# Kernel optimization log

Measured on AMD Instinct MI355X. Metric: run time of the kernel, lower is better.

## Reference

```python
import jax, jax.numpy as jnp
import numpy as np

EPS = 1e-5
K = 3  # deformable conv kernel size


def _conv2d_same(x, w, b=None):
    # x (N,C,H,W), w (O,I,kh,kw), stride 1, SAME padding
    y = jax.lax.conv_general_dilated(
        x, w, window_strides=(1, 1), padding='SAME',
        dimension_numbers=('NCHW', 'OIHW', 'NCHW'))
    if b is not None:
        y = y + b[None, :, None, None]
    return y


def _bilinear_sample(x, ys, xs):
    # x (N,C,H,W); ys, xs (N,H,W) float sample coords -> (N,C,H,W), zero pad outside
    N, C, H, W = x.shape
    y0 = jnp.floor(ys)
    x0 = jnp.floor(xs)
    dy = ys - y0
    dx = xs - x0
    xf = x.reshape(N, C, H * W)

    def gather(yi, xi):
        valid = (yi >= 0) & (yi < H) & (xi >= 0) & (xi < W)
        yc = jnp.clip(yi, 0, H - 1).astype(jnp.int32)
        xc = jnp.clip(xi, 0, W - 1).astype(jnp.int32)
        idx = (yc * W + xc).reshape(N, 1, H * W)
        v = jnp.take_along_axis(xf, jnp.broadcast_to(idx, (N, C, H * W)), axis=2)
        return v.reshape(N, C, H, W) * valid[:, None].astype(x.dtype)

    v00 = gather(y0, x0)
    v01 = gather(y0, x0 + 1)
    v10 = gather(y0 + 1, x0)
    v11 = gather(y0 + 1, x0 + 1)
    dy = dy[:, None]
    dx = dx[:, None]
    return (v00 * (1 - dy) * (1 - dx) + v01 * (1 - dy) * dx
            + v10 * dy * (1 - dx) + v11 * dy * dx)


def _dcn_v2(x, w_off, b_off, w, b):
    # Modulated deformable conv (DCNv2), 3x3, stride 1, pad 1
    N, Cin, H, W = x.shape
    om = _conv2d_same(x, w_off, b_off)              # (N, 3*K*K, H, W)
    o1, o2, m = jnp.split(om, 3, axis=1)
    off = jnp.concatenate([o1, o2], axis=1)          # (N, 2*K*K, H, W)
    mask = jax.nn.sigmoid(m)                         # (N, K*K, H, W)
    base_y = jnp.arange(H, dtype=x.dtype)[None, :, None]  # (1,H,1)
    base_x = jnp.arange(W, dtype=x.dtype)[None, None, :]  # (1,1,W)
    out = jnp.broadcast_to(b[None, :, None, None], (N, w.shape[0], H, W)).astype(x.dtype)
    for k in range(K * K):  # fixed small loop over kernel taps
        ki, kj = k // K, k % K
        ys = base_y + (ki - 1) + off[:, 2 * k]
        xs = base_x + (kj - 1) + off[:, 2 * k + 1]
        v = _bilinear_sample(x, ys, xs) * mask[:, k][:, None]
        out = out + jnp.einsum('nchw,oc->nohw', v, w[:, :, ki, kj])
    return out


def _batchnorm(x, gamma, beta):
    # training-mode BN over (N,H,W)
    mu = x.mean(axis=(0, 2, 3), keepdims=True)
    var = x.var(axis=(0, 2, 3), keepdims=True)
    xhat = (x - mu) * jax.lax.rsqrt(var + EPS)
    return xhat * gamma[None, :, None, None] + beta[None, :, None, None]


def _conv_transpose2d(x, w):
    # torch ConvTranspose2d(k=4, s=2, p=1, bias=False); w (Cin, Cout, 4, 4)
    kernel = jnp.flip(w, (2, 3)).transpose(1, 0, 2, 3)  # (Cout, Cin, 4, 4)
    return jax.lax.conv_general_dilated(
        x, kernel, window_strides=(1, 1),
        padding=((2, 2), (2, 2)), lhs_dilation=(2, 2),
        dimension_numbers=('NCHW', 'OIHW', 'NCHW'))


def setup_inputs() -> dict:
    key = jax.random.key(0)
    ks = jax.random.split(key, 9)
    N, inC, outC, H, W = 8, 256, 256, 64, 64
    x = jax.random.normal(ks[0], (N, inC, H, W), dtype=jnp.float32)
    w_off = jax.random.normal(ks[1], (3 * K * K, inC, K, K), dtype=jnp.float32) * 0.01
    b_off = jnp.zeros((3 * K * K,), dtype=jnp.float32)
    w_dcn = jax.random.normal(ks[2], (outC, inC, K, K), dtype=jnp.float32) * (1.0 / np.sqrt(inC * K * K))
    b_dcn = jnp.zeros((outC,), dtype=jnp.float32)
    gamma1 = jnp.ones((outC,), dtype=jnp.float32)
    beta1 = jnp.zeros((outC,), dtype=jnp.float32)
    w_ct = jax.random.normal(ks[3], (outC, outC, 4, 4), dtype=jnp.float32) * (1.0 / np.sqrt(outC * 16))
    gamma2 = jnp.ones((outC,), dtype=jnp.float32)
    beta2 = jnp.zeros((outC,), dtype=jnp.float32)
    return {'x': x, 'w_off': w_off, 'b_off': b_off, 'w_dcn': w_dcn,
            'b_dcn': b_dcn, 'gamma1': gamma1, 'beta1': beta1,
            'w_ct': w_ct, 'gamma2': gamma2, 'beta2': beta2}


def reference(x, w_off, b_off, w_dcn, b_dcn, gamma1, beta1, w_ct, gamma2, beta2):
    out = _dcn_v2(x, w_off, b_off, w_dcn, b_dcn)
    out = jax.nn.relu(_batchnorm(out, gamma1, beta1))
    out = _conv_transpose2d(out, w_ct)
    out = jax.nn.relu(_batchnorm(out, gamma2, beta2))
    return out  # (N, outC, 2H, 2W)
```

## Files before the change

kernel.cpp:

```cpp
#include <hip/hip_runtime.h>


#define OFF_XT   0u
#define SZ_XT    (8u*64u*64u*256u)
#define OFF_Y1   (OFF_XT + SZ_XT)
#define SZ_Y1    SZ_XT
#define OFF_OM   (OFF_Y1 + SZ_Y1)
#define SZ_OM    (8u*27u*4096u)
#define OFF_WD   (OFF_OM + SZ_OM)
#define SZ_WD    (9u*256u*256u)
#define OFF_WC   (OFF_WD + SZ_WD)
#define SZ_WC    (16u*256u*256u)
#define OFF_WO   (OFF_WC + 524288u)
#define OFF_P1   (OFF_WC + 565248u)
#define OFF_ST   (OFF_WC + SZ_WC)

typedef __attribute__((ext_vector_type(8))) short bf16x8;
typedef __attribute__((ext_vector_type(4))) float f32x4;

__device__ __forceinline__ unsigned short f2bf(float f) {
  unsigned int u = __float_as_uint(f);
  u += 0x7fffu + ((u >> 16) & 1u);
  return (unsigned short)(u >> 16);
}

__device__ __forceinline__ unsigned int lerp_pair(unsigned int u00, unsigned int u01,
                                                  unsigned int u10, unsigned int u11,
                                                  float w0, float w1, float w2, float w3) {
  float lo = w0 * __uint_as_float(u00 << 16) + w1 * __uint_as_float(u01 << 16) +
             w2 * __uint_as_float(u10 << 16) + w3 * __uint_as_float(u11 << 16);
  float hi = w0 * __uint_as_float(u00 & 0xffff0000u) + w1 * __uint_as_float(u01 & 0xffff0000u) +
             w2 * __uint_as_float(u10 & 0xffff0000u) + w3 * __uint_as_float(u11 & 0xffff0000u);
  return (unsigned int)f2bf(lo) | ((unsigned int)f2bf(hi) << 16);
}

__device__ __forceinline__ unsigned int norm_pair(unsigned int u, float scx, float shx,
                                                  float scy, float shy) {
  float lo = fmaxf(fmaf(__uint_as_float(u << 16), scx, shx), 0.f);
  float hi = fmaxf(fmaf(__uint_as_float(u & 0xffff0000u), scy, shy), 0.f);
  return (unsigned int)f2bf(lo) | ((unsigned int)f2bf(hi) << 16);
}

__global__ __launch_bounds__(256) void k_transpose_x(const float* __restrict__ x,
                                                     unsigned short* __restrict__ xtb) {
  __shared__ float tile[32][33];
  int ny = blockIdx.x;
  int n = ny >> 6, y = ny & 63;
  int c0 = blockIdx.y * 32;
  int w0 = blockIdx.z * 32;
  int t = threadIdx.x;
  int tx = t & 31, ty = t >> 5;
#pragma unroll
  for (int i = 0; i < 4; ++i) {
    int c = c0 + ty + i * 8;
    tile[ty + i * 8][tx] = x[(((n * 256 + c) * 64 + y) << 6) + w0 + tx];
  }
  __syncthreads();
#pragma unroll
  for (int i = 0; i < 4; ++i) {
    int wl = ty + i * 8;
    xtb[(((n * 64 + y) * 64 + (w0 + wl)) << 8) + c0 + tx] = f2bf(tile[tx][wl]);
  }
}

__global__ void k_prep_wdcn(const float* __restrict__ w, unsigned short* __restrict__ wdb) {
  int idx = blockIdx.x * 256 + threadIdx.x;
  if (idx < 589824) {
    int cil = idx & 31;
    int co = (idx >> 5) & 255;
    int chunk = (idx >> 13) & 7;
    int k = idx >> 16;
    int ci = chunk * 32 + cil;
    wdb[idx] = f2bf(w[(co * 256 + ci) * 9 + k]);
  }
}

__global__ void k_prep_wct(const float* __restrict__ w, unsigned short* __restrict__ wcb) {
  int idx = blockIdx.x * 256 + threadIdx.x;
  int cil = idx & 31;
  int co = (idx >> 5) & 255;
  int chunk = (idx >> 13) & 7;
  int tap = (idx >> 16) & 3;
  int px = (idx >> 18) & 1;
  int py = (idx >> 19) & 1;
  int ci = chunk * 32 + cil;
  int krA = (py == 0) ? 3 : 2, krB = (py == 0) ? 1 : 0;
  int kc0 = (px == 0) ? 3 : 2, kc1 = kc0 - 2;
  int kr = (tap < 2) ? krA : krB;
  int kc = (tap & 1) ? kc1 : kc0;
  float v = w[(ci << 12) + (co << 4) + kr * 4 + kc];
  wcb[idx] = f2bf(v);
}

__global__ void k_prep_woff(const float* __restrict__ w, unsigned short* __restrict__ wob) {
  int idx = blockIdx.x * 256 + threadIdx.x;
  int cil = idx & 31;
  int co = (idx >> 5) & 31;
  int chunk = (idx >> 10) & 7;
  int tap = idx >> 13;
  int ci = chunk * 32 + cil;
  float v = (co < 27) ? w[(co * 256 + ci) * 9 + tap] : 0.f;
  wob[idx] = f2bf(v);
}

__global__ __launch_bounds__(512) void k_offset_mfma(const unsigned short* __restrict__ xtb,
                                                     const unsigned short* __restrict__ wob,
                                                     const float* __restrict__ b_off,
                                                     float* __restrict__ om) {
  __shared__ unsigned short aLds[6 * 66 * 40];
  __shared__ unsigned short wLds[9 * 32 * 40];
  int bid = blockIdx.x;
  int n = bid & 7, yq = bid >> 3;
  int ybase = yq * 4;
  int t = threadIdx.x;
  int wave = t >> 6, lane = t & 63;
  int lr = wave >> 1, cb = (wave & 1) * 32;
  int l15 = lane & 15, l4 = lane >> 4;
  f32x4 acc[2][2] = {};

  for (int chunk = 0; chunk < 8; ++chunk) {
    __syncthreads();
    for (int task = t; task < 1584; task += 512) {
      int slot = task & 3;
      int rc = task >> 2;
      int c = rc % 66, r = rc / 66;
      int gy = ybase - 1 + r, gx = c - 1;
      uint4 val = make_uint4(0u, 0u, 0u, 0u);
      if (gy >= 0 && gy < 64 && gx >= 0 && gx < 64)
        val = *(const uint4*)&xtb[((size_t)(n * 4096 + gy * 64 + gx) << 8) + chunk * 32 + slot * 8];
      *(uint4*)&aLds[(r * 66 + c) * 40 + slot * 8] = val;
    }
    for (int task = t; task < 1152; task += 512) {
      int sl = task & 3;
      int co = (task >> 2) & 31;
      int tap = task >> 7;
      *(uint4*)&wLds[(tap * 32 + co) * 40 + sl * 8] =
          *(const uint4*)&wob[(size_t)((tap * 8 + chunk) * 32 + co) * 32 + sl * 8];
    }
    __syncthreads();
#pragma unroll
    for (int ky = 0; ky < 3; ++ky)
#pragma unroll
      for (int kx = 0; kx < 3; ++kx) {
        int tap = ky * 3 + kx;
        bf16x8 b0 = *(bf16x8*)&wLds[(tap * 32 + l15) * 40 + l4 * 8];
        bf16x8 b1 = *(bf16x8*)&wLds[(tap * 32 + 16 + l15) * 40 + l4 * 8];
        bf16x8 a0 = *(bf16x8*)&aLds[((lr + ky) * 66 + cb + l15 + kx) * 40 + l4 * 8];
        bf16x8 a1 = *(bf16x8*)&aLds[((lr + ky) * 66 + cb + 16 + l15 + kx) * 40 + l4 * 8];
        acc[0][0] = __builtin_amdgcn_mfma_f32_16x16x32_bf16(a0, b0, acc[0][0], 0, 0, 0);
        acc[0][1] = __builtin_amdgcn_mfma_f32_16x16x32_bf16(a0, b1, acc[0][1], 0, 0, 0);
        acc[1][0] = __builtin_amdgcn_mfma_f32_16x16x32_bf16(a1, b0, acc[1][0], 0, 0, 0);
        acc[1][1] = __builtin_amdgcn_mfma_f32_16x16x32_bf16(a1, b1, acc[1][1], 0, 0, 0);
      }
  }
  int row = ybase + lr;
#pragma unroll
  for (int j = 0; j < 2; ++j) {
    int co = 16 * j + l15;
    if (co < 27) {
      float bias = b_off[co];
      float* dst = om + ((size_t)(n * 27 + co) << 12) + row * 64;
#pragma unroll
      for (int i = 0; i < 2; ++i) {
        f32x4 v = acc[i][j];
        float4 o = make_float4(v[0] + bias, v[1] + bias, v[2] + bias, v[3] + bias);
        *(float4*)&dst[cb + 16 * i + l4 * 4] = o;
      }
    }
  }
}

__global__ __launch_bounds__(512) void k_dcn2(const unsigned short* __restrict__ xtb,
                                              const float* __restrict__ om,
                                              const unsigned short* __restrict__ wdb,
                                              const float* __restrict__ b_dcn,
                                              unsigned short* __restrict__ y1r,
                                              float* __restrict__ part1) {
  __shared__ unsigned short aLds[2][128 * 40];
  __shared__ int p_yx[1152];
  __shared__ float p_w[1152 * 4];
  __shared__ float sstat[512];
  int bid = blockIdx.x;
  int n = bid & 7, yp = bid >> 3;
  int ybase = yp * 2;
  int t = threadIdx.x;
  int wave = t >> 6, lane = t & 63;
  int mh = wave >> 2, ns = wave & 3;
  int l15 = lane & 15, l4 = lane >> 4;
  int gp = t >> 2, gq = t & 3;
  int nb = n << 12;
  f32x4 acc[4][4] = {};

  for (int i = t; i < 1152; i += 512) {
    int tap = i >> 7, pp = i & 127;
    int ki = tap / 3, kj = tap % 3;
    int yy = ybase + (pp >> 6), xx = pp & 63;
    const float* base = om + (n * 27) * 4096 + (yy << 6) + xx;
    float offy = base[(2 * tap) * 4096];
    float offx = base[(2 * tap + 1) * 4096];
    float mv = base[(18 + tap) * 4096];
    float mask = 1.f / (1.f + expf(-mv));
    float ysf = (float)(yy + ki - 1) + offy;
    float xsf = (float)(xx + kj - 1) + offx;
    float y0f = floorf(ysf), x0f = floorf(xsf);
    float dy = ysf - y0f, dx = xsf - x0f;
    int y0 = (int)y0f, x0 = (int)x0f;
    int y1c = y0 + 1, x1c = x0 + 1;
    float v00 = (y0 >= 0 && y0 < 64 && x0 >= 0 && x0 < 64) ? 1.f : 0.f;
    float v01 = (y0 >= 0 && y0 < 64 && x1c >= 0 && x1c < 64) ? 1.f : 0.f;
    float v10 = (y1c >= 0 && y1c < 64 && x0 >= 0 && x0 < 64) ? 1.f : 0.f;
    float v11 = (y1c >= 0 && y1c < 64 && x1c >= 0 && x1c < 64) ? 1.f : 0.f;
    int cy0 = min(max(y0, 0), 63), cy1 = min(max(y1c, 0), 63);
    int cx0 = min(max(x0, 0), 63), cx1 = min(max(x1c, 0), 63);
    p_yx[i] = cy0 | (cy1 << 8) | (cx0 << 16) | (cx1 << 24);
    p_w[i * 4 + 0] = (1.f - dy) * (1.f - dx) * mask * v00;
    p_w[i * 4 + 1] = (1.f - dy) * dx * mask * v01;
    p_w[i * 4 + 2] = dy * (1.f - dx) * mask * v10;
    p_w[i * 4 + 3] = dy * dx * mask * v11;
  }
  __syncthreads();

  const unsigned short *b00, *b01, *b10, *b11;
  float w0, w1, w2, w3;
#define LOADP(TAP_)                                                                   \
  {                                                                                   \
    int ii = (TAP_) * 128 + gp;                                                       \
    int pk = p_yx[ii];                                                                \
    int y0 = pk & 255, y1c = (pk >> 8) & 255, x0 = (pk >> 16) & 255, x1c = pk >> 24;  \
    w0 = p_w[ii * 4 + 0]; w1 = p_w[ii * 4 + 1];                                       \
    w2 = p_w[ii * 4 + 2]; w3 = p_w[ii * 4 + 3];                                       \
    b00 = xtb + ((size_t)(nb + (y0 << 6) + x0) << 8) + gq * 8;                        \
    b01 = xtb + ((size_t)(nb + (y0 << 6) + x1c) << 8) + gq * 8;                       \
    b10 = xtb + ((size_t)(nb + (y1c << 6) + x0) << 8) + gq * 8;                       \
    b11 = xtb + ((size_t)(nb + (y1c << 6) + x1c) << 8) + gq * 8;                      \
  }
#define WRITE_A(BUF_)                                                                 \
  {                                                                                   \
    uint4 o;                                                                          \
    o.x = lerp_pair(g00.x, g01.x, g10.x, g11.x, w0, w1, w2, w3);                      \
    o.y = lerp_pair(g00.y, g01.y, g10.y, g11.y, w0, w1, w2, w3);                      \
    o.z = lerp_pair(g00.z, g01.z, g10.z, g11.z, w0, w1, w2, w3);                      \
    o.w = lerp_pair(g00.w, g01.w, g10.w, g11.w, w0, w1, w2, w3);                      \
    *(uint4*)&aLds[BUF_][gp * 40 + gq * 8] = o;                                       \
  }
  uint4 g00, g01, g10, g11;
  LOADP(0);
  g00 = *(const uint4*)(b00); g01 = *(const uint4*)(b01);
  g10 = *(const uint4*)(b10); g11 = *(const uint4*)(b11);
  WRITE_A(0);
  g00 = *(const uint4*)(b00 + 32); g01 = *(const uint4*)(b01 + 32);
  g10 = *(const uint4*)(b10 + 32); g11 = *(const uint4*)(b11 + 32);
  __syncthreads();

  for (int p = 0; p < 72; ++p) {
    int cur = p & 1;
    int tap = p >> 3, chunk = p & 7;
    const unsigned short* wp = wdb + (size_t)tap * 65536 + chunk * 8192;
    bf16x8 b[4], a[4];
#pragma unroll
    for (int j = 0; j < 4; ++j)
      b[j] = *(bf16x8*)&wp[(ns * 64 + 16 * j + l15) * 32 + l4 * 8];
#pragma unroll
    for (int i = 0; i < 4; ++i)
      a[i] = *(bf16x8*)&aLds[cur][(mh * 64 + 16 * i + l15) * 40 + l4 * 8];
#pragma unroll
    for (int i = 0; i < 4; ++i)
#pragma unroll
      for (int j = 0; j < 4; ++j)
        acc[i][j] = __builtin_amdgcn_mfma_f32_16x16x32_bf16(a[i], b[j], acc[i][j], 0, 0, 0);
    if (p < 71) {
      WRITE_A(cur ^ 1);
      int q = p + 2;
      if (q < 72) {
        int qt = q >> 3, qc = q & 7;
        if (qc == 0) LOADP(qt);
        int cio = qc * 32;
        g00 = *(const uint4*)(b00 + cio); g01 = *(const uint4*)(b01 + cio);
        g10 = *(const uint4*)(b10 + cio); g11 = *(const uint4*)(b11 + cio);
      }
    }
    __syncthreads();
  }
#undef LOADP
#undef WRITE_A
  sstat[t] = 0.f;
  __syncthreads();
  unsigned short* dst = y1r + ((size_t)(n * 4096 + ybase * 64) << 8);
#pragma unroll
  for (int j = 0; j < 4; ++j) {
    int co = ns * 64 + 16 * j + l15;
    float bias = b_dcn[co];
    float ss = 0.f, qq = 0.f;
#pragma unroll
    for (int i = 0; i < 4; ++i)
#pragma unroll
      for (int rr = 0; rr < 4; ++rr) {
        int pos = mh * 64 + 16 * i + l4 * 4 + rr;
        float v = acc[i][j][rr] + bias;
        dst[pos * 256 + co] = f2bf(v);
        ss += v; qq += v * v;
      }
    ss += __shfl_xor(ss, 16); ss += __shfl_xor(ss, 32);
    qq += __shfl_xor(qq, 16); qq += __shfl_xor(qq, 32);
    if (l4 == 0) { atomicAdd(&sstat[co], ss); atomicAdd(&sstat[256 + co], qq); }
  }
  __syncthreads();
  part1[(size_t)bid * 512 + t] = sstat[t];
}

__global__ __launch_bounds__(256) void k_finalize_p(const float* __restrict__ part,
                                                    const float* __restrict__ gamma,
                                                    const float* __restrict__ beta,
                                                    float* __restrict__ scsh,
                                                    float inv_cnt, int nblocks) {
  __shared__ float red[512];
  int c = blockIdx.x;
  int t = threadIdx.x;
  float s = 0.f, q = 0.f;
  for (int b = t; b < nblocks; b += 256) {
    s += part[(size_t)b * 512 + c];
    q += part[(size_t)b * 512 + 256 + c];
  }
  red[t] = s;
  red[256 + t] = q;
  __syncthreads();
  for (int w = 128; w > 0; w >>= 1) {
    if (t < w) { red[t] += red[t + w]; red[256 + t] += red[256 + t + w]; }
    __syncthreads();
  }
  if (t == 0) {
    float mu = red[0] * inv_cnt;
    float var = red[256] * inv_cnt - mu * mu;
    float r = rsqrtf(var + 1e-5f);
    float sc = gamma[c] * r;
    scsh[c] = sc;
    scsh[256 + c] = beta[c] - mu * sc;
  }
}

__global__ __launch_bounds__(512) void k_convt2(const unsigned short* __restrict__ y1b,
                                               const unsigned short* __restrict__ wcb,
                                               const float* __restrict__ scsh1,
                                               float* __restrict__ out,
                                               float* __restrict__ part2) {
  __shared__ unsigned short sh[16896];
  __shared__ float sstat[512];
  unsigned short* aLds = sh;

  int bid = blockIdx.x;
  int n = bid & 7;
  int r2 = bid >> 3;
  int py = r2 & 1;
  int ub = r2 >> 1;
  int u0 = ub * 2;
  int ry0 = u0 - 1 + py;
  int t = threadIdx.x;
  int wave = t >> 6, lane = t & 63;
  int px_w = wave >> 2, ns = wave & 3;
  int co_base = ns * 64;
  int l15 = lane & 15, l4 = lane >> 4;
  bool rvalid[3];
#pragma unroll
  for (int r = 0; r < 3; ++r) rvalid[r] = (ry0 + r >= 0) && (ry0 + r < 64);

  f32x4 acc[2][4][4] = {};

  for (int chunk = 0; chunk < 8; ++chunk) {
    int ci0 = chunk * 32;
    __syncthreads();
    for (int task = t; task < 792; task += 512) {
      int slot = task & 3;
      int rc = task >> 2;
      int c = rc % 66;
      int r = rc / 66;
      int ix = c - 1;
      uint4 val = make_uint4(0u, 0u, 0u, 0u);
      if (rvalid[r] && ix >= 0 && ix < 64) {
        uint4 raw = *(const uint4*)&y1b[((size_t)(n * 4096 + (ry0 + r) * 64 + ix) * 256 + ci0 + slot * 8)];
        int cb = ci0 + slot * 8;
        float4 sc0 = *(const float4*)&scsh1[cb];
        float4 sc1 = *(const float4*)&scsh1[cb + 4];
        float4 sh0 = *(const float4*)&scsh1[256 + cb];
        float4 sh1 = *(const float4*)&scsh1[256 + cb + 4];
        val.x = norm_pair(raw.x, sc0.x, sh0.x, sc0.y, sh0.y);
        val.y = norm_pair(raw.y, sc0.z, sh0.z, sc0.w, sh0.w);
        val.z = norm_pair(raw.z, sc1.x, sh1.x, sc1.y, sh1.y);
        val.w = norm_pair(raw.w, sc1.z, sh1.z, sc1.w, sh1.w);
      }
      *(uint4*)&aLds[(r * 66 + c) * 40 + slot * 8] = val;
    }
    __syncthreads();
    for (int tap = 0; tap < 4; ++tap) {
      int r_ofs = tap >> 1, s = tap & 1;
      const unsigned short* wsrc =
          wcb + ((size_t)((((py * 2 + px_w) * 4 + tap) * 8 + chunk) * 256 + co_base)) * 32;
      bf16x8 b[4];
#pragma unroll
      for (int j = 0; j < 4; ++j)
        b[j] = *(bf16x8*)&wsrc[(16 * j + l15) * 32 + l4 * 8];
#pragma unroll
      for (int k = 0; k < 2; ++k)
#pragma unroll
        for (int i = 0; i < 4; ++i) {
          int c = 16 * i + l15 + s + px_w;
          bf16x8 a = *(bf16x8*)&aLds[((k + r_ofs) * 66 + c) * 40 + l4 * 8];
#pragma unroll
          for (int j = 0; j < 4; ++j)
            acc[k][i][j] = __builtin_amdgcn_mfma_f32_16x16x32_bf16(a, b[j], acc[k][i][j], 0, 0, 0);
        }
    }
  }

  sstat[t] = 0.f;
  float* epi = (float*)sh;
#pragma unroll
  for (int k = 0; k < 2; ++k) {
    int oy = 2 * (u0 + k) + py;
    for (int qt = 0; qt < 4; ++qt) {
      __syncthreads();
      if (ns == qt) {
#pragma unroll
        for (int i = 0; i < 4; ++i)
#pragma unroll
          for (int j = 0; j < 4; ++j) {
            int co_l = 16 * j + l15;
            int vbase = 16 * i + l4 * 4;
            *(f32x4*)&epi[co_l * 132 + px_w * 64 + vbase] = acc[k][i][j];
          }
      }
      __syncthreads();
#pragma unroll
      for (int it = 0; it < 4; ++it) {
        int task = it * 512 + t;
        int q = task & 31;
        int co_l = task >> 5;
        int co = qt * 64 + co_l;
        float e00 = epi[co_l * 132 + 2 * q];
        float e01 = epi[co_l * 132 + 2 * q + 1];
        float e10 = epi[co_l * 132 + 64 + 2 * q];
        float e11 = epi[co_l * 132 + 64 + 2 * q + 1];
        float4 vv = make_float4(e00, e10, e01, e11);
        *(float4*)&out[((size_t)(n * 256 + co) * 128 + oy) * 128 + 4 * q] = vv;
        float ss = e00 + e01 + e10 + e11;
        float qq = e00 * e00 + e01 * e01 + e10 * e10 + e11 * e11;
        ss += __shfl_xor(ss, 1);  qq += __shfl_xor(qq, 1);
        ss += __shfl_xor(ss, 2);  qq += __shfl_xor(qq, 2);
        ss += __shfl_xor(ss, 4);  qq += __shfl_xor(qq, 4);
        ss += __shfl_xor(ss, 8);  qq += __shfl_xor(qq, 8);
        ss += __shfl_xor(ss, 16); qq += __shfl_xor(qq, 16);
        if ((lane & 31) == 0) {
          atomicAdd(&sstat[co], ss);
          atomicAdd(&sstat[256 + co], qq);
        }
      }
    }
  }
  __syncthreads();
  part2[(size_t)bid * 512 + t] = sstat[t];
}

__global__ void k_norm_nchw(float* __restrict__ buf, const float* __restrict__ scsh) {
  int idx = blockIdx.x * 256 + threadIdx.x;
  int c = (idx >> 12) & 255;
  float sc = scsh[c], sh = scsh[256 + c];
  float4 v = *(float4*)&buf[(size_t)idx * 4];
  v.x = fmaxf(fmaf(v.x, sc, sh), 0.f);
  v.y = fmaxf(fmaf(v.y, sc, sh), 0.f);
  v.z = fmaxf(fmaf(v.z, sc, sh), 0.f);
  v.w = fmaxf(fmaf(v.w, sc, sh), 0.f);
  *(float4*)&buf[(size_t)idx * 4] = v;
}

extern "C" void kernel_launch(void* const* d_in, const int* in_sizes, int n_in,
                              void* d_out, int out_size, void* d_ws, size_t ws_size,
                              hipStream_t stream) {
  (void)in_sizes; (void)n_in; (void)out_size; (void)ws_size;
  const float* x      = (const float*)d_in[0];
  const float* w_off  = (const float*)d_in[1];
  const float* b_off  = (const float*)d_in[2];
  const float* w_dcn  = (const float*)d_in[3];
  const float* b_dcn  = (const float*)d_in[4];
  const float* gamma1 = (const float*)d_in[5];
  const float* beta1  = (const float*)d_in[6];
  const float* w_ct   = (const float*)d_in[7];
  const float* gamma2 = (const float*)d_in[8];
  const float* beta2  = (const float*)d_in[9];
  float* ws  = (float*)d_ws;
  unsigned short* xtb = (unsigned short*)(ws + OFF_XT);
  unsigned short* y1r = (unsigned short*)(ws + OFF_Y1);
  float* om  = ws + OFF_OM;
  unsigned short* wdb = (unsigned short*)(ws + OFF_WD);
  unsigned short* wcb = (unsigned short*)(ws + OFF_WC);
  unsigned short* wob = (unsigned short*)(ws + OFF_WO);
  float* st  = ws + OFF_ST;
  float* p1  = ws + OFF_P1;
  float* out = (float*)d_out;

  k_transpose_x<<<dim3(512, 8, 2), 256, 0, stream>>>(x, xtb);
  k_prep_wdcn<<<2304, 256, 0, stream>>>(w_dcn, wdb);
  k_prep_wct<<<4096, 256, 0, stream>>>(w_ct, wcb);
  k_prep_woff<<<288, 256, 0, stream>>>(w_off, wob);
  k_offset_mfma<<<128, 512, 0, stream>>>(xtb, wob, b_off, om);
  k_dcn2<<<256, 512, 0, stream>>>(xtb, om, wdb, b_dcn, y1r, p1);
  k_finalize_p<<<256, 256, 0, stream>>>(p1, gamma1, beta1, st + 512, 1.f / 32768.f, 256);
  k_convt2<<<512, 512, 0, stream>>>(y1r, wcb, st + 512, out, om);
  k_finalize_p<<<256, 256, 0, stream>>>(om, gamma2, beta2, st + 1536, 1.f / 131072.f, 512);
  k_norm_nchw<<<32768, 256, 0, stream>>>(out, st + 1536);
}
```

Measured before the change: 257.0 us.

## Double-buffer conv-transpose input tiles with register prefetch across chunks

The k_convt2 A-tile staging loop is replaced by a double-buffered LDS scheme. Global loads for chunk+2 are issued into registers while chunk+1 is normalized and written into the alternate buffer after the MFMAs of the current chunk. Per-thread addresses and validity masks are computed once outside the loop instead of per task. This aims to hide global load latency and drop one barrier per chunk, at the cost of more registers and two LDS buffers (2×7920 shorts) that must still fit in the existing 16896-short array.

After: 248.5 us, median of 2. 3.3% less time.

```diff
diff --git a/kernel.cpp b/kernel.cpp
--- a/kernel.cpp
+++ b/kernel.cpp
@@ -345,7 +345,6 @@
                                                float* __restrict__ part2) {
   __shared__ unsigned short sh[16896];
   __shared__ float sstat[512];
-  unsigned short* aLds = sh;
 
   int bid = blockIdx.x;
   int n = bid & 7;
@@ -359,37 +358,66 @@
   int px_w = wave >> 2, ns = wave & 3;
   int co_base = ns * 64;
   int l15 = lane & 15, l4 = lane >> 4;
-  bool rvalid[3];
-#pragma unroll
-  for (int r = 0; r < 3; ++r) rvalid[r] = (ry0 + r >= 0) && (ry0 + r < 64);
+
+  int as0 = t & 3, arc0 = t >> 2, ac0 = arc0 % 66, ar0 = arc0 / 66;
+  int t2 = t + 512;
+  int as1 = t2 & 3, arc1 = t2 >> 2, ac1 = arc1 % 66, ar1 = arc1 / 66;
+  bool a1v = (t < 280);
+  size_t nbase = (size_t)n * 4096;
+  int ry_0 = ry0 + ar0, ry_1 = ry0 + ar1;
+  bool av0 = (ry_0 >= 0) && (ry_0 < 64) && (ac0 - 1) >= 0 && (ac0 - 1) < 64;
+  bool av1 = a1v && (ry_1 >= 0) && (ry_1 < 64) && (ac1 - 1) >= 0 && (ac1 - 1) < 64;
+  const unsigned short* asrc0 = y1b + (nbase + (size_t)ry_0 * 64 + (ac0 - 1)) * 256 + as0 * 8;
+  const unsigned short* asrc1 = y1b + (nbase + (size_t)ry_1 * 64 + (ac1 - 1)) * 256 + as1 * 8;
+  int aoff0 = (ar0 * 66 + ac0) * 40 + as0 * 8;
+  int aoff1 = (ar1 * 66 + ac1) * 40 + as1 * 8;
 
   f32x4 acc[2][4][4] = {};
 
+  uint4 raw0, raw1;
+#define NORMWRITE(BUF_, CHUNK_)                                                          \
+  {                                                                                      \
+    unsigned short* ab = sh + (BUF_)*7920;                                               \
+    int cb0 = (CHUNK_)*32 + as0 * 8;                                                     \
+    uint4 val = make_uint4(0u, 0u, 0u, 0u);                                              \
+    if (av0) {                                                                           \
+      float4 sc0 = *(const float4*)&scsh1[cb0];                                          \
+      float4 sc1 = *(const float4*)&scsh1[cb0 + 4];                                      \
+      float4 sh0 = *(const float4*)&scsh1[256 + cb0];                                    \
+      float4 sh1 = *(const float4*)&scsh1[256 + cb0 + 4];                                \
+      val.x = norm_pair(raw0.x, sc0.x, sh0.x, sc0.y, sh0.y);                             \
+      val.y = norm_pair(raw0.y, sc0.z, sh0.z, sc0.w, sh0.w);                             \
+      val.z = norm_pair(raw0.z, sc1.x, sh1.x, sc1.y, sh1.y);                             \
+      val.w = norm_pair(raw0.w, sc1.z, sh1.z, sc1.w, sh1.w);                             \
+    }                                                                                    \
+    *(uint4*)&ab[aoff0] = val;                                                           \
+    if (a1v) {                                                                           \
+      int cb1 = (CHUNK_)*32 + as1 * 8;                                                   \
+      uint4 v1 = make_uint4(0u, 0u, 0u, 0u);                                             \
+      if (av1) {                                                                         \
+        float4 sc0 = *(const float4*)&scsh1[cb1];                                        \
+        float4 sc1 = *(const float4*)&scsh1[cb1 + 4];                                    \
+        float4 sh0 = *(const float4*)&scsh1[256 + cb1];                                  \
+        float4 sh1 = *(const float4*)&scsh1[256 + cb1 + 4];                              \
+        v1.x = norm_pair(raw1.x, sc0.x, sh0.x, sc0.y, sh0.y);                            \
+        v1.y = norm_pair(raw1.y, sc0.z, sh0.z, sc0.w, sh0.w);                            \
+        v1.z = norm_pair(raw1.z, sc1.x, sh1.x, sc1.y, sh1.y);                            \
+        v1.w = norm_pair(raw1.w, sc1.z, sh1.z, sc1.w, sh1.w);                            \
+      }                                                                                  \
+      *(uint4*)&ab[aoff1] = v1;                                                          \
+    }                                                                                    \
+  }
+
+  raw0 = av0 ? *(const uint4*)(asrc0) : make_uint4(0u, 0u, 0u, 0u);
+  raw1 = av1 ? *(const uint4*)(asrc1) : make_uint4(0u, 0u, 0u, 0u);
+  NORMWRITE(0, 0);
+  raw0 = av0 ? *(const uint4*)(asrc0 + 32) : make_uint4(0u, 0u, 0u, 0u);
+  raw1 = av1 ? *(const uint4*)(asrc1 + 32) : make_uint4(0u, 0u, 0u, 0u);
+  __syncthreads();
+
   for (int chunk = 0; chunk < 8; ++chunk) {
-    int ci0 = chunk * 32;
-    __syncthreads();
-    for (int task = t; task < 792; task += 512) {
-      int slot = task & 3;
-      int rc = task >> 2;
-      int c = rc % 66;
-      int r = rc / 66;
-      int ix = c - 1;
-      uint4 val = make_uint4(0u, 0u, 0u, 0u);
-      if (rvalid[r] && ix >= 0 && ix < 64) {
-        uint4 raw = *(const uint4*)&y1b[((size_t)(n * 4096 + (ry0 + r) * 64 + ix) * 256 + ci0 + slot * 8)];
-        int cb = ci0 + slot * 8;
-        float4 sc0 = *(const float4*)&scsh1[cb];
-        float4 sc1 = *(const float4*)&scsh1[cb + 4];
-        float4 sh0 = *(const float4*)&scsh1[256 + cb];
-        float4 sh1 = *(const float4*)&scsh1[256 + cb + 4];
-        val.x = norm_pair(raw.x, sc0.x, sh0.x, sc0.y, sh0.y);
-        val.y = norm_pair(raw.y, sc0.z, sh0.z, sc0.w, sh0.w);
-        val.z = norm_pair(raw.z, sc1.x, sh1.x, sc1.y, sh1.y);
-        val.w = norm_pair(raw.w, sc1.z, sh1.z, sc1.w, sh1.w);
-      }
-      *(uint4*)&aLds[(r * 66 + c) * 40 + slot * 8] = val;
-    }
-    __syncthreads();
+    int cur = chunk & 1;
+    const unsigned short* abuf = sh + cur * 7920;
     for (int tap = 0; tap < 4; ++tap) {
       int r_ofs = tap >> 1, s = tap & 1;
       const unsigned short* wsrc =
@@ -403,13 +431,23 @@
 #pragma unroll
         for (int i = 0; i < 4; ++i) {
           int c = 16 * i + l15 + s + px_w;
-          bf16x8 a = *(bf16x8*)&aLds[((k + r_ofs) * 66 + c) * 40 + l4 * 8];
+          bf16x8 a = *(bf16x8*)&abuf[((k + r_ofs) * 66 + c) * 40 + l4 * 8];
 #pragma unroll
           for (int j = 0; j < 4; ++j)
             acc[k][i][j] = __builtin_amdgcn_mfma_f32_16x16x32_bf16(a, b[j], acc[k][i][j], 0, 0, 0);
         }
     }
-  }
+    if (chunk < 7) {
+      NORMWRITE(cur ^ 1, chunk + 1);
+      if (chunk < 6) {
+        int nc = (chunk + 2) * 32;
+        raw0 = av0 ? *(const uint4*)(asrc0 + nc) : make_uint4(0u, 0u, 0u, 0u);
+        raw1 = av1 ? *(const uint4*)(asrc1 + nc) : make_uint4(0u, 0u, 0u, 0u);
+      }
+    }
+    __syncthreads();
+  }
+#undef NORMWRITE
 
   sstat[t] = 0.f;
   float* epi = (float*)sh;
```
